# Optimization experiments

Hardware: AMD Instinct MI355X
Metric: run time of the kernel (lower is better)

Reference implementation:

```python
import jax, jax.numpy as jnp
import numpy as np

N_NODES = 100000
N_EDGES = 600000
N_GRAPHS = 5000
IN_DIM = 11
HID = 128
EDGE_DIM = 3
N_REST = 4  # layers 1..4
BN_EPS = 1e-5


def setup_inputs() -> dict:
    key = jax.random.key(0)
    ks = iter(jax.random.split(key, 40))
    s = 0.05
    inp = {}
    inp['x'] = jax.random.normal(next(ks), (N_NODES, IN_DIM), dtype=jnp.float32)
    inp['edge_attr'] = jax.random.normal(next(ks), (N_EDGES, EDGE_DIM), dtype=jnp.float32)
    # layer 0 (input_dim -> hidden)
    inp['e_w0'] = jax.random.normal(next(ks), (EDGE_DIM, IN_DIM), dtype=jnp.float32) * s
    inp['e_b0'] = jnp.zeros((IN_DIM,), jnp.float32)
    inp['w1_0'] = jax.random.normal(next(ks), (IN_DIM, HID), dtype=jnp.float32) * s
    inp['b1_0'] = jnp.zeros((HID,), jnp.float32)
    inp['w2_0'] = jax.random.normal(next(ks), (HID, HID), dtype=jnp.float32) * s
    inp['b2_0'] = jnp.zeros((HID,), jnp.float32)
    inp['gamma0'] = jnp.ones((HID,), jnp.float32)
    inp['beta0'] = jnp.zeros((HID,), jnp.float32)
    inp['eps0'] = jnp.zeros((), jnp.float32)
    # layers 1..4 stacked
    inp['e_w'] = jax.random.normal(next(ks), (N_REST, EDGE_DIM, HID), dtype=jnp.float32) * s
    inp['e_b'] = jnp.zeros((N_REST, HID), jnp.float32)
    inp['w1'] = jax.random.normal(next(ks), (N_REST, HID, HID), dtype=jnp.float32) * s
    inp['b1'] = jnp.zeros((N_REST, HID), jnp.float32)
    inp['w2'] = jax.random.normal(next(ks), (N_REST, HID, HID), dtype=jnp.float32) * s
    inp['b2'] = jnp.zeros((N_REST, HID), jnp.float32)
    inp['gamma'] = jnp.ones((N_REST, HID), jnp.float32)
    inp['beta'] = jnp.zeros((N_REST, HID), jnp.float32)
    inp['eps_r'] = jnp.zeros((N_REST,), jnp.float32)
    # head MLP
    inp['hw1'] = jax.random.normal(next(ks), (HID, HID), dtype=jnp.float32) * s
    inp['hb1'] = jnp.zeros((HID,), jnp.float32)
    inp['hw2'] = jax.random.normal(next(ks), (HID, HID), dtype=jnp.float32) * s
    inp['hb2'] = jnp.zeros((HID,), jnp.float32)
    inp['hw3'] = jax.random.normal(next(ks), (HID, 1), dtype=jnp.float32) * s
    inp['hb3'] = jnp.zeros((1,), jnp.float32)
    # graph structure (int constants)
    inp['edge_index'] = jax.random.randint(next(ks), (2, N_EDGES), 0, N_NODES, dtype=jnp.int32)
    inp['batch'] = jnp.sort(jax.random.randint(next(ks), (N_NODES,), 0, N_GRAPHS, dtype=jnp.int32))
    return inp


def _gine_layer(x, src, dst, edge_attr, e_w, e_b, eps, w1, b1, w2, b2, gamma, beta):
    # message = relu(x_j + Linear(edge_attr)); aggregate = scatter-add on dst
    msg = jax.nn.relu(x[src] + edge_attr @ e_w + e_b)            # [E, d]
    aggr = jax.ops.segment_sum(msg, dst, num_segments=N_NODES)  # [N, d]
    h = (1.0 + eps) * x + aggr
    h = jax.nn.relu(h @ w1 + b1) @ w2 + b2                       # GIN MLP
    mu = h.mean(axis=0)
    var = h.var(axis=0)  # biased, as torch BN training-mode normalization
    h = (h - mu) * jax.lax.rsqrt(var + BN_EPS) * gamma + beta
    return jax.nn.relu(h)


def reference(x, edge_attr, e_w0, e_b0, w1_0, b1_0, w2_0, b2_0, gamma0, beta0, eps0,
              e_w, e_b, w1, b1, w2, b2, gamma, beta, eps_r,
              hw1, hb1, hw2, hb2, hw3, hb3, edge_index, batch):
    src, dst = edge_index[0], edge_index[1]
    # layer 0: input_dim -> hidden, no residual (dims differ)
    h = _gine_layer(x, src, dst, edge_attr, e_w0, e_b0, eps0,
                    w1_0, b1_0, w2_0, b2_0, gamma0, beta0)
    # layers 1..4: hidden -> hidden, with residual
    for i in range(N_REST):
        h_res = h
        h = _gine_layer(h, src, dst, edge_attr, e_w[i], e_b[i], eps_r[i],
                        w1[i], b1[i], w2[i], b2[i], gamma[i], beta[i])
        h = h + h_res
    # global mean pool per graph
    sums = jax.ops.segment_sum(h, batch, num_segments=N_GRAPHS)
    cnts = jax.ops.segment_sum(jnp.ones((h.shape[0],), h.dtype), batch, num_segments=N_GRAPHS)
    pooled = sums / jnp.maximum(cnts, 1.0)[:, None]
    # head MLP (dropout = eval no-op)
    z = jax.nn.relu(pooled @ hw1 + hb1)
    z = jax.nn.relu(z @ hw2 + hb2)
    return z @ hw3 + hb3
```

## Files before the change

kernel.cpp:

```cpp
#include <hip/hip_runtime.h>
#include <hip/hip_fp16.h>

#define N_NODES 100000
#define N_EDGES 600000
#define N_GRAPHS 5000
#define IN_DIM 11
#define HID 128
#define NREST 4
#define BN_EPS 1e-5f
#define SCAN_BS 256
#define NBLK ((N_NODES + SCAN_BS - 1) / SCAN_BS)
#define WSLOT 16384

typedef __bf16 bf16x8 __attribute__((ext_vector_type(8)));
typedef float f32x4 __attribute__((ext_vector_type(4)));

__device__ inline bf16x8 as_bf16x8(uint4 u) { return __builtin_bit_cast(bf16x8, u); }

__device__ inline void split_bf16(float x, unsigned short& hi, unsigned short& lo) {
    unsigned int b = __float_as_uint(x);
    hi = (unsigned short)(b >> 16);
    float rem = x - __uint_as_float(b & 0xFFFF0000u);
    lo = (unsigned short)(__float_as_uint(rem) >> 16);
}

__device__ inline uint4 pack8(const unsigned short* h) {
    uint4 u;
    u.x = (unsigned)h[0] | ((unsigned)h[1] << 16);
    u.y = (unsigned)h[2] | ((unsigned)h[3] << 16);
    u.z = (unsigned)h[4] | ((unsigned)h[5] << 16);
    u.w = (unsigned)h[6] | ((unsigned)h[7] << 16);
    return u;
}

__global__ void k_zero(int* deg, int* gstart, int* gend, float* stats) {
    int i = blockIdx.x * 256 + threadIdx.x;
    if (i < N_NODES) deg[i] = 0;
    if (i < N_GRAPHS) { gstart[i] = 0; gend[i] = 0; }
    if (i < 5 * 2 * HID) stats[i] = 0.f;
}

__global__ void k_deg(const int* __restrict__ ei, int* __restrict__ deg) {
    int e = blockIdx.x * 256 + threadIdx.x;
    if (e < N_EDGES) atomicAdd(&deg[ei[N_EDGES + e]], 1);
}

__global__ void k_scan_a(const int* __restrict__ deg, int* __restrict__ rowstart,
                         int* __restrict__ bsum) {
    __shared__ int sh[SCAN_BS];
    int t = threadIdx.x, i = blockIdx.x * SCAN_BS + t;
    int v = (i < N_NODES) ? deg[i] : 0;
    sh[t] = v;
    __syncthreads();
    for (int off = 1; off < SCAN_BS; off <<= 1) {
        int add = (t >= off) ? sh[t - off] : 0;
        __syncthreads();
        sh[t] += add;
        __syncthreads();
    }
    if (i < N_NODES) rowstart[i] = sh[t] - v;
    if (t == SCAN_BS - 1) bsum[blockIdx.x] = sh[t];
}

__global__ void k_scan_b(const int* __restrict__ bsum, int* __restrict__ boff) {
    __shared__ int sh[512];
    int t = threadIdx.x;
    int v = (t < NBLK) ? bsum[t] : 0;
    sh[t] = v;
    __syncthreads();
    for (int off = 1; off < 512; off <<= 1) {
        int add = (t >= off) ? sh[t - off] : 0;
        __syncthreads();
        sh[t] += add;
        __syncthreads();
    }
    if (t < NBLK) boff[t] = sh[t] - v;
}

__global__ void k_scan_c(int* __restrict__ rowstart, const int* __restrict__ boff,
                         int* __restrict__ cur) {
    int i = blockIdx.x * 256 + threadIdx.x;
    if (i < N_NODES) {
        int v = rowstart[i] + boff[i / SCAN_BS];
        rowstart[i] = v;
        cur[i] = v;
    }
    if (i == 0) rowstart[N_NODES] = N_EDGES;
}

__global__ void k_fill(const int* __restrict__ ei, const float* __restrict__ ea,
                       int* __restrict__ cur, uint4* __restrict__ csr_pack) {
    int e = blockIdx.x * 256 + threadIdx.x;
    if (e < N_EDGES) {
        int d = ei[N_EDGES + e];
        int p = atomicAdd(&cur[d], 1);
        uint4 pk;
        pk.x = (unsigned)ei[e];
        pk.y = __float_as_uint(ea[3 * e + 0]);
        pk.z = __float_as_uint(ea[3 * e + 1]);
        pk.w = __float_as_uint(ea[3 * e + 2]);
        csr_pack[p] = pk;
    }
}

__global__ void k_pack(const float* __restrict__ w1_0, const float* __restrict__ w2_0,
                       const float* __restrict__ w1, const float* __restrict__ w2,
                       unsigned short* __restrict__ Whi, unsigned short* __restrict__ Wlo) {
    int bid = blockIdx.x;
    int slot = bid >> 5;
    int kc = (bid >> 3) & 3, cb = bid & 7;
    int lane = threadIdx.x;
    const float* src;
    int K;
    if (slot == 0) { src = w1_0; K = IN_DIM; }
    else if (slot == 1) { src = w2_0; K = HID; }
    else if (slot < 6) { src = w1 + (size_t)(slot - 2) * HID * HID; K = HID; }
    else { src = w2 + (size_t)(slot - 6) * HID * HID; K = HID; }
    int col = cb * 16 + (lane & 15);
    int kbase = kc * 32 + 8 * (lane >> 4);
    unsigned short hi[8], lo[8];
#pragma unroll
    for (int j = 0; j < 8; ++j) {
        int k = kbase + j;
        float v = (k < K) ? src[(size_t)k * HID + col] : 0.f;
        split_bf16(v, hi[j], lo[j]);
    }
    size_t base = ((size_t)bid * 64 + lane) * 8;
    *(uint4*)(Whi + base) = pack8(hi);
    *(uint4*)(Wlo + base) = pack8(lo);
}

__global__ void k_agg0(const float* __restrict__ x, const int* __restrict__ rowstart,
                       const uint4* __restrict__ csr_pack,
                       const float* __restrict__ ew, const float* __restrict__ eb,
                       const float* __restrict__ epsp, float* __restrict__ Z0) {
    int wave = (blockIdx.x * blockDim.x + threadIdx.x) >> 6;
    int lane = threadIdx.x & 63;
    if (wave >= N_NODES) return;
    int n = wave;
    int slot = lane >> 4;
    int c = lane & 15;
    int cc = (c < IN_DIM) ? c : 0;
    float w0 = ew[cc], w1 = ew[IN_DIM + cc], w2 = ew[2 * IN_DIM + cc];
    float bb = eb[cc];
    float acc = 0.f;
    int i0 = rowstart[n], i1 = rowstart[n + 1];
    int i = i0 + slot;
    uint4 pk;
    if (i < i1) pk = csr_pack[i];
    while (i < i1) {
        int inext = i + 4;
        uint4 pknext;
        if (inext < i1) pknext = csr_pack[inext];
        int s = (int)pk.x;
        float m = x[s * IN_DIM + cc] + __uint_as_float(pk.y) * w0 +
                  __uint_as_float(pk.z) * w1 + __uint_as_float(pk.w) * w2 + bb;
        acc += fmaxf(m, 0.f);
        pk = pknext;
        i = inext;
    }
    acc += __shfl_xor(acc, 16, 64);
    acc += __shfl_xor(acc, 32, 64);
    if (lane < IN_DIM) {
        float epsv = 1.0f + epsp[0];
        Z0[n * IN_DIM + lane] = epsv * x[n * IN_DIM + lane] + acc;
    }
}

__global__ __launch_bounds__(256, 4) void k_agg128(
        const float* __restrict__ h, const __half* __restrict__ hh,
        const int* __restrict__ rowstart, const uint4* __restrict__ csr_pack,
        const float* __restrict__ ew, const float* __restrict__ eb,
        const float* __restrict__ epsp, int layer, float* __restrict__ Z) {
    int wave = (blockIdx.x * blockDim.x + threadIdx.x) >> 6;
    int lane = threadIdx.x & 63;
    if (wave >= N_NODES) return;
    int n = wave;
    int slot = lane >> 4;
    int c = (lane & 15) * 8;
    float4 w0a = *(const float4*)(ew + 0 * HID + c), w0b = *(const float4*)(ew + 0 * HID + c + 4);
    float4 w1a = *(const float4*)(ew + 1 * HID + c), w1b = *(const float4*)(ew + 1 * HID + c + 4);
    float4 w2a = *(const float4*)(ew + 2 * HID + c), w2b = *(const float4*)(ew + 2 * HID + c + 4);
    float4 bba = *(const float4*)(eb + c),           bbb = *(const float4*)(eb + c + 4);
    float a0 = 0.f, a1 = 0.f, a2 = 0.f, a3 = 0.f, a4 = 0.f, a5 = 0.f, a6 = 0.f, a7 = 0.f;
    int i0 = rowstart[n], i1 = rowstart[n + 1];
    int i = i0 + slot;
    uint4 pk;
    if (i < i1) pk = csr_pack[i];
    while (i < i1) {
        int inext = i + 4;
        uint4 pknext;
        if (inext < i1) pknext = csr_pack[inext];
        int s = (int)pk.x;
        float ea0 = __uint_as_float(pk.y);
        float ea1 = __uint_as_float(pk.z);
        float ea2 = __uint_as_float(pk.w);
        uint4 hv = *(const uint4*)(hh + (size_t)s * HID + c);
        float2 f0 = __half22float2(__builtin_bit_cast(__half2, hv.x));
        float2 f1 = __half22float2(__builtin_bit_cast(__half2, hv.y));
        float2 f2 = __half22float2(__builtin_bit_cast(__half2, hv.z));
        float2 f3 = __half22float2(__builtin_bit_cast(__half2, hv.w));
        a0 += fmaxf(f0.x + ea0 * w0a.x + ea1 * w1a.x + ea2 * w2a.x + bba.x, 0.f);
        a1 += fmaxf(f0.y + ea0 * w0a.y + ea1 * w1a.y + ea2 * w2a.y + bba.y, 0.f);
        a2 += fmaxf(f1.x + ea0 * w0a.z + ea1 * w1a.z + ea2 * w2a.z + bba.z, 0.f);
        a3 += fmaxf(f1.y + ea0 * w0a.w + ea1 * w1a.w + ea2 * w2a.w + bba.w, 0.f);
        a4 += fmaxf(f2.x + ea0 * w0b.x + ea1 * w1b.x + ea2 * w2b.x + bbb.x, 0.f);
        a5 += fmaxf(f2.y + ea0 * w0b.y + ea1 * w1b.y + ea2 * w2b.y + bbb.y, 0.f);
        a6 += fmaxf(f3.x + ea0 * w0b.z + ea1 * w1b.z + ea2 * w2b.z + bbb.z, 0.f);
        a7 += fmaxf(f3.y + ea0 * w0b.w + ea1 * w1b.w + ea2 * w2b.w + bbb.w, 0.f);
        pk = pknext;
        i = inext;
    }
#pragma unroll
    for (int m = 16; m <= 32; m <<= 1) {
        a0 += __shfl_xor(a0, m, 64); a1 += __shfl_xor(a1, m, 64);
        a2 += __shfl_xor(a2, m, 64); a3 += __shfl_xor(a3, m, 64);
        a4 += __shfl_xor(a4, m, 64); a5 += __shfl_xor(a5, m, 64);
        a6 += __shfl_xor(a6, m, 64); a7 += __shfl_xor(a7, m, 64);
    }
    if (slot == 0) {
        float epsv = 1.0f + epsp[layer];
        float4 hna = *(const float4*)(h + (size_t)n * HID + c);
        float4 hnb = *(const float4*)(h + (size_t)n * HID + c + 4);
        float4 za, zb;
        za.x = epsv * hna.x + a0; za.y = epsv * hna.y + a1;
        za.z = epsv * hna.z + a2; za.w = epsv * hna.w + a3;
        zb.x = epsv * hnb.x + a4; zb.y = epsv * hnb.y + a5;
        zb.z = epsv * hnb.z + a6; zb.w = epsv * hnb.w + a7;
        *(float4*)(Z + (size_t)n * HID + c) = za;
        *(float4*)(Z + (size_t)n * HID + c + 4) = zb;
    }
}

template <int K1>
__global__ __launch_bounds__(256, 4) void k_mlp(const float* Zin,
        const unsigned short* __restrict__ W1hi, const unsigned short* __restrict__ W1lo,
        const unsigned short* __restrict__ W2hi, const unsigned short* __restrict__ W2lo,
        const float* __restrict__ B1, const float* __restrict__ B2,
        float* Hpre, float* __restrict__ stats) {
    constexpr int KC1 = (K1 == 128) ? 4 : 1;
    __shared__ __align__(16) unsigned short ahi[4 * 4 * 64 * 8];
    __shared__ __align__(16) unsigned short alo[4 * 4 * 64 * 8];
    __shared__ float red[1024];
    const int tid = threadIdx.x;
    const int w = tid >> 6;
    const int l = tid & 63;
    const int row0 = blockIdx.x * 64;

    if (K1 == 128) {
#pragma unroll
        for (int it = 0; it < 4; ++it) {
            int s = tid + it * 256;
            int lane = s & 63, kc = (s >> 6) & 3, wr = s >> 8;
            int r = row0 + wr * 16 + (lane & 15);
            int k0 = kc * 32 + 8 * (lane >> 4);
            float v[8];
            if (r < N_NODES) {
                *(float4*)(v) = *(const float4*)(Zin + (size_t)r * 128 + k0);
                *(float4*)(v + 4) = *(const float4*)(Zin + (size_t)r * 128 + k0 + 4);
            } else {
#pragma unroll
                for (int j = 0; j < 8; ++j) v[j] = 0.f;
            }
            unsigned short h[8], q[8];
#pragma unroll
            for (int j = 0; j < 8; ++j) split_bf16(v[j], h[j], q[j]);
            *(uint4*)(ahi + (size_t)s * 8) = pack8(h);
            *(uint4*)(alo + (size_t)s * 8) = pack8(q);
        }
    } else {
        int lane = tid & 63, wr = tid >> 6;
        int r = row0 + wr * 16 + (lane & 15);
        int k0 = 8 * (lane >> 4);
        float v[8];
#pragma unroll
        for (int j = 0; j < 8; ++j) {
            int k = k0 + j;
            v[j] = (r < N_NODES && k < IN_DIM) ? Zin[(size_t)r * IN_DIM + k] : 0.f;
        }
        unsigned short h[8], q[8];
#pragma unroll
        for (int j = 0; j < 8; ++j) split_bf16(v[j], h[j], q[j]);
        size_t s = (size_t)(wr * 4 + 0) * 64 + lane;
        *(uint4*)(ahi + s * 8) = pack8(h);
        *(uint4*)(alo + s * 8) = pack8(q);
    }
    __syncthreads();

    const int cb0 = 2 * w, cb1 = cb0 + 1;
    const f32x4 zf = {0.f, 0.f, 0.f, 0.f};

    f32x4 acc[4][2];
#pragma unroll
    for (int wr = 0; wr < 4; ++wr) { acc[wr][0] = zf; acc[wr][1] = zf; }

#pragma unroll
    for (int kc = 0; kc < KC1; ++kc) {
        bf16x8 bh0 = as_bf16x8(*(const uint4*)(W1hi + ((size_t)(kc * 8 + cb0) * 64 + l) * 8));
        bf16x8 bl0 = as_bf16x8(*(const uint4*)(W1lo + ((size_t)(kc * 8 + cb0) * 64 + l) * 8));
        bf16x8 bh1 = as_bf16x8(*(const uint4*)(W1hi + ((size_t)(kc * 8 + cb1) * 64 + l) * 8));
        bf16x8 bl1 = as_bf16x8(*(const uint4*)(W1lo + ((size_t)(kc * 8 + cb1) * 64 + l) * 8));
#pragma unroll
        for (int wr = 0; wr < 4; ++wr) {
            bf16x8 a_h = as_bf16x8(*(const uint4*)(ahi + ((size_t)(wr * 4 + kc) * 64 + l) * 8));
            bf16x8 a_l = as_bf16x8(*(const uint4*)(alo + ((size_t)(wr * 4 + kc) * 64 + l) * 8));
            acc[wr][0] = __builtin_amdgcn_mfma_f32_16x16x32_bf16(a_h, bh0, acc[wr][0], 0, 0, 0);
            acc[wr][1] = __builtin_amdgcn_mfma_f32_16x16x32_bf16(a_h, bh1, acc[wr][1], 0, 0, 0);
            acc[wr][0] = __builtin_amdgcn_mfma_f32_16x16x32_bf16(a_l, bh0, acc[wr][0], 0, 0, 0);
            acc[wr][1] = __builtin_amdgcn_mfma_f32_16x16x32_bf16(a_l, bh1, acc[wr][1], 0, 0, 0);
            acc[wr][0] = __builtin_amdgcn_mfma_f32_16x16x32_bf16(a_h, bl0, acc[wr][0], 0, 0, 0);
            acc[wr][1] = __builtin_amdgcn_mfma_f32_16x16x32_bf16(a_h, bl1, acc[wr][1], 0, 0, 0);
        }
    }
    __syncthreads();

    {
        float b1c0 = B1[cb0 * 16 + (l & 15)];
        float b1c1 = B1[cb1 * 16 + (l & 15)];
        int j2 = l & 7;
        int hi16 = (l & 15) >> 3;
        int l2r = (l >> 4) * 4;
#pragma unroll
        for (int wr = 0; wr < 4; ++wr) {
#pragma unroll
            for (int cbl = 0; cbl < 2; ++cbl) {
                float bv = cbl ? b1c1 : b1c0;
                f32x4 v = acc[wr][cbl];
#pragma unroll
                for (int r = 0; r < 4; ++r) {
                    float t = fmaxf(v[r] + bv, 0.f);
                    unsigned short hh, qq;
                    split_bf16(t, hh, qq);
                    int l2 = l2r + r + 16 * (2 * cbl + hi16);
                    int off = ((wr * 4 + w) * 64 + l2) * 8 + j2;
                    ahi[off] = hh;
                    alo[off] = qq;
                }
            }
        }
    }
    __syncthreads();

    f32x4 acc2[4][2];
#pragma unroll
    for (int wr = 0; wr < 4; ++wr) { acc2[wr][0] = zf; acc2[wr][1] = zf; }

#pragma unroll
    for (int kc = 0; kc < 4; ++kc) {
        bf16x8 bh0 = as_bf16x8(*(const uint4*)(W2hi + ((size_t)(kc * 8 + cb0) * 64 + l) * 8));
        bf16x8 bl0 = as_bf16x8(*(const uint4*)(W2lo + ((size_t)(kc * 8 + cb0) * 64 + l) * 8));
        bf16x8 bh1 = as_bf16x8(*(const uint4*)(W2hi + ((size_t)(kc * 8 + cb1) * 64 + l) * 8));
        bf16x8 bl1 = as_bf16x8(*(const uint4*)(W2lo + ((size_t)(kc * 8 + cb1) * 64 + l) * 8));
#pragma unroll
        for (int wr = 0; wr < 4; ++wr) {
            bf16x8 a_h = as_bf16x8(*(const uint4*)(ahi + ((size_t)(wr * 4 + kc) * 64 + l) * 8));
            bf16x8 a_l = as_bf16x8(*(const uint4*)(alo + ((size_t)(wr * 4 + kc) * 64 + l) * 8));
            acc2[wr][0] = __builtin_amdgcn_mfma_f32_16x16x32_bf16(a_h, bh0, acc2[wr][0], 0, 0, 0);
            acc2[wr][1] = __builtin_amdgcn_mfma_f32_16x16x32_bf16(a_h, bh1, acc2[wr][1], 0, 0, 0);
            acc2[wr][0] = __builtin_amdgcn_mfma_f32_16x16x32_bf16(a_l, bh0, acc2[wr][0], 0, 0, 0);
            acc2[wr][1] = __builtin_amdgcn_mfma_f32_16x16x32_bf16(a_l, bh1, acc2[wr][1], 0, 0, 0);
            acc2[wr][0] = __builtin_amdgcn_mfma_f32_16x16x32_bf16(a_h, bl0, acc2[wr][0], 0, 0, 0);
            acc2[wr][1] = __builtin_amdgcn_mfma_f32_16x16x32_bf16(a_h, bl1, acc2[wr][1], 0, 0, 0);
        }
    }

    {
        float b2c0 = B2[cb0 * 16 + (l & 15)];
        float b2c1 = B2[cb1 * 16 + (l & 15)];
        float s0 = 0.f, q0 = 0.f, s1 = 0.f, q1 = 0.f;
#pragma unroll
        for (int wr = 0; wr < 4; ++wr) {
#pragma unroll
            for (int r = 0; r < 4; ++r) {
                int grow = row0 + wr * 16 + (l >> 4) * 4 + r;
                if (grow < N_NODES) {
                    float o0 = acc2[wr][0][r] + b2c0;
                    float o1 = acc2[wr][1][r] + b2c1;
                    Hpre[(size_t)grow * 128 + cb0 * 16 + (l & 15)] = o0;
                    Hpre[(size_t)grow * 128 + cb1 * 16 + (l & 15)] = o1;
                    s0 += o0; q0 += o0 * o0;
                    s1 += o1; q1 += o1 * o1;
                }
            }
        }
        red[(w * 2 + 0) * 64 + l] = s0;
        red[(w * 2 + 1) * 64 + l] = s1;
        red[512 + (w * 2 + 0) * 64 + l] = q0;
        red[512 + (w * 2 + 1) * 64 + l] = q1;
    }
    __syncthreads();
    if (tid < 128) {
        int b = ((tid >> 5) * 2 + ((tid >> 4) & 1)) * 64 + (tid & 15);
        float ss = red[b] + red[b + 16] + red[b + 32] + red[b + 48];
        float qq = red[512 + b] + red[512 + b + 16] + red[512 + b + 32] + red[512 + b + 48];
        atomicAdd(&stats[tid], ss);
        atomicAdd(&stats[128 + tid], qq);
    }
}

__global__ void k_bn(const float* __restrict__ Hpre, const float* __restrict__ stats,
                     const float* __restrict__ gamma, const float* __restrict__ beta,
                     float* __restrict__ h, __half* __restrict__ hh, int residual) {
    int idx = blockIdx.x * 256 + threadIdx.x;
    const float invN = 1.f / (float)N_NODES;
    int c4 = idx & 31;
    float4 v = ((const float4*)Hpre)[idx];
    float4 s0 = ((const float4*)stats)[c4];
    float4 s1 = ((const float4*)(stats + 128))[c4];
    float4 g = ((const float4*)gamma)[c4];
    float4 bt = ((const float4*)beta)[c4];
    float4 r;
    {
        float mu = s0.x * invN, var = s1.x * invN - mu * mu;
        r.x = fmaxf((v.x - mu) * rsqrtf(var + BN_EPS) * g.x + bt.x, 0.f);
    }
    {
        float mu = s0.y * invN, var = s1.y * invN - mu * mu;
        r.y = fmaxf((v.y - mu) * rsqrtf(var + BN_EPS) * g.y + bt.y, 0.f);
    }
    {
        float mu = s0.z * invN, var = s1.z * invN - mu * mu;
        r.z = fmaxf((v.z - mu) * rsqrtf(var + BN_EPS) * g.z + bt.z, 0.f);
    }
    {
        float mu = s0.w * invN, var = s1.w * invN - mu * mu;
        r.w = fmaxf((v.w - mu) * rsqrtf(var + BN_EPS) * g.w + bt.w, 0.f);
    }
    if (residual) {
        float4 hv = ((const float4*)h)[idx];
        r.x += hv.x; r.y += hv.y; r.z += hv.z; r.w += hv.w;
    }
    ((float4*)h)[idx] = r;
    if (hh) {
        __half2 p0 = __floats2half2_rn(r.x, r.y);
        __half2 p1 = __floats2half2_rn(r.z, r.w);
        uint2 pk;
        pk.x = __builtin_bit_cast(unsigned int, p0);
        pk.y = __builtin_bit_cast(unsigned int, p1);
        *(uint2*)(hh + (size_t)idx * 4) = pk;
    }
}

__global__ void k_bounds(const int* __restrict__ batch, int* __restrict__ gstart,
                         int* __restrict__ gend) {
    int r = blockIdx.x * 256 + threadIdx.x;
    if (r >= N_NODES) return;
    int b = batch[r];
    if (r == 0 || batch[r - 1] != b) gstart[b] = r;
    if (r == N_NODES - 1 || batch[r + 1] != b) gend[b] = r + 1;
}

__global__ void k_pool(const float* __restrict__ h, const int* __restrict__ gstart,
                       const int* __restrict__ gend, float* __restrict__ pooled) {
    int wave = (blockIdx.x * blockDim.x + threadIdx.x) >> 6;
    int lane = threadIdx.x & 63;
    if (wave >= N_GRAPHS) return;
    int g = wave;
    int c = lane * 2;
    int a = gstart[g], b = gend[g];
    float ax = 0.f, ay = 0.f;
    for (int r = a; r < b; ++r) {
        float2 v = *(const float2*)(h + (size_t)r * HID + c);
        ax += v.x;
        ay += v.y;
    }
    float d = fmaxf((float)(b - a), 1.f);
    float2 o;
    o.x = ax / d;
    o.y = ay / d;
    *(float2*)(pooled + (size_t)g * HID + c) = o;
}

__global__ void k_head(const float* __restrict__ pooled, const float* __restrict__ hw1,
                       const float* __restrict__ hb1, const float* __restrict__ hw2,
                       const float* __restrict__ hb2, const float* __restrict__ hw3,
                       const float* __restrict__ hb3, float* __restrict__ out) {
    __shared__ float ps[2][128];
    __shared__ float t1s[2][128];
    __shared__ float red[256];
    int tid = threadIdx.x;
    int rr = tid >> 7, c = tid & 127;
    int row = blockIdx.x * 2 + rr;
    ps[rr][c] = pooled[(size_t)row * 128 + c];
    __syncthreads();
    float a = hb1[c];
    for (int k = 0; k < 128; ++k) a = fmaf(ps[rr][k], hw1[k * 128 + c], a);
    t1s[rr][c] = fmaxf(a, 0.f);
    __syncthreads();
    float b = hb2[c];
    for (int k = 0; k < 128; ++k) b = fmaf(t1s[rr][k], hw2[k * 128 + c], b);
    b = fmaxf(b, 0.f);
    red[tid] = b * hw3[c];
    for (int s = 64; s > 0; s >>= 1) {
        __syncthreads();
        if (c < s) red[tid] += red[tid + s];
    }
    __syncthreads();
    if (c == 0) out[row] = red[tid] + hb3[0];
}

extern "C" void kernel_launch(void* const* d_in, const int* in_sizes, int n_in,
                              void* d_out, int out_size, void* d_ws, size_t ws_size,
                              hipStream_t stream) {
    const float* x = (const float*)d_in[0];
    const float* edge_attr = (const float*)d_in[1];
    const float* e_w0 = (const float*)d_in[2];
    const float* e_b0 = (const float*)d_in[3];
    const float* w1_0 = (const float*)d_in[4];
    const float* b1_0 = (const float*)d_in[5];
    const float* w2_0 = (const float*)d_in[6];
    const float* b2_0 = (const float*)d_in[7];
    const float* gamma0 = (const float*)d_in[8];
    const float* beta0 = (const float*)d_in[9];
    const float* eps0 = (const float*)d_in[10];
    const float* e_w = (const float*)d_in[11];
    const float* e_b = (const float*)d_in[12];
    const float* w1 = (const float*)d_in[13];
    const float* b1 = (const float*)d_in[14];
    const float* w2 = (const float*)d_in[15];
    const float* b2 = (const float*)d_in[16];
    const float* gamma = (const float*)d_in[17];
    const float* beta = (const float*)d_in[18];
    const float* eps_r = (const float*)d_in[19];
    const float* hw1 = (const float*)d_in[20];
    const float* hb1 = (const float*)d_in[21];
    const float* hw2 = (const float*)d_in[22];
    const float* hb2 = (const float*)d_in[23];
    const float* hw3 = (const float*)d_in[24];
    const float* hb3 = (const float*)d_in[25];
    const int* edge_index = (const int*)d_in[26];
    const int* batch = (const int*)d_in[27];
    float* out = (float*)d_out;

    float* wsf = (float*)d_ws;
    size_t off = 0;
    float* A = wsf + off;      off += (size_t)N_NODES * HID;
    float* ZB = wsf + off;     off += (size_t)N_NODES * HID;
    float* Z0 = wsf + off;     off += (size_t)N_NODES * IN_DIM;
    float* pooled = wsf + off; off += (size_t)N_GRAPHS * HID;
    float* stats = wsf + off;  off += 5 * 2 * HID;
    __half* hhalf = (__half*)(wsf + off); off += (size_t)N_NODES * HID / 2;
    int* ib = (int*)(wsf + off);
    uint4* csr_pack = (uint4*)ib;
    size_t io = 4 * (size_t)N_EDGES;
    int* deg = ib + io;      io += N_NODES;
    int* rowstart = ib + io; io += N_NODES + 4;
    int* cur = ib + io;      io += N_NODES;
    int* gstart = ib + io;   io += N_GRAPHS;
    int* gend = ib + io;     io += N_GRAPHS;
    int* bsum = ib + io;     io += 512;
    int* boff = ib + io;     io += 512;
    unsigned short* Whi = (unsigned short*)(ib + io);
    unsigned short* Wlo = Whi + 10 * WSLOT;

    const int EB = (N_EDGES + 255) / 256;
    const int NB = (N_NODES + 255) / 256;
    const int MLPB = (N_NODES + 63) / 64;

    k_zero<<<NB, 256, 0, stream>>>(deg, gstart, gend, stats);
    k_pack<<<320, 64, 0, stream>>>(w1_0, w2_0, w1, w2, Whi, Wlo);

    k_deg<<<EB, 256, 0, stream>>>(edge_index, deg);
    k_scan_a<<<NBLK, SCAN_BS, 0, stream>>>(deg, rowstart, bsum);
    k_scan_b<<<1, 512, 0, stream>>>(bsum, boff);
    k_scan_c<<<NB, 256, 0, stream>>>(rowstart, boff, cur);
    k_fill<<<EB, 256, 0, stream>>>(edge_index, edge_attr, cur, csr_pack);

    k_agg0<<<(N_NODES * 64) / 256, 256, 0, stream>>>(x, rowstart, csr_pack, e_w0,
                                                     e_b0, eps0, Z0);
    k_mlp<IN_DIM><<<MLPB, 256, 0, stream>>>(Z0, Whi + 0 * WSLOT, Wlo + 0 * WSLOT,
                                            Whi + 1 * WSLOT, Wlo + 1 * WSLOT,
                                            b1_0, b2_0, ZB, stats);
    k_bn<<<(N_NODES * HID / 4) / 256, 256, 0, stream>>>(ZB, stats, gamma0, beta0, A,
                                                        hhalf, 0);

    for (int i = 0; i < NREST; ++i) {
        k_agg128<<<(N_NODES * 64) / 256, 256, 0, stream>>>(
            A, hhalf, rowstart, csr_pack, e_w + (size_t)i * 3 * HID,
            e_b + (size_t)i * HID, eps_r, i, ZB);
        k_mlp<HID><<<MLPB, 256, 0, stream>>>(ZB, Whi + (size_t)(2 + i) * WSLOT,
                                             Wlo + (size_t)(2 + i) * WSLOT,
                                             Whi + (size_t)(6 + i) * WSLOT,
                                             Wlo + (size_t)(6 + i) * WSLOT,
                                             b1 + (size_t)i * HID, b2 + (size_t)i * HID,
                                             ZB, stats + (size_t)(i + 1) * 2 * HID);
        k_bn<<<(N_NODES * HID / 4) / 256, 256, 0, stream>>>(
            ZB, stats + (size_t)(i + 1) * 2 * HID, gamma + (size_t)i * HID,
            beta + (size_t)i * HID, A, (i < NREST - 1) ? hhalf : (__half*)nullptr, 1);
    }

    k_bounds<<<NB, 256, 0, stream>>>(batch, gstart, gend);
    k_pool<<<(N_GRAPHS * 64) / 256, 256, 0, stream>>>(A, gstart, gend, pooled);
    k_head<<<N_GRAPHS / 2, 256, 0, stream>>>(pooled, hw1, hb1, hw2, hb2, hw3, hb3, out);
}
```

Before: 920.3 us.

## Store node features only in fp16, ping-pong buffers, drop fp32 copy

Removes the fp32 node-feature buffer. k_bn now writes only fp16 output, reads the fp16 residual from the previous buffer, and processes 8 elements per thread. k_agg128 and k_pool read the self term and pooled values from fp16, and two fp16 buffers alternate between layers. The manual software prefetch in the aggregation loops is replaced with plain loops. This cuts the memory traffic of BN, the self read and pooling, but carrying the residual stream in fp16 lets rounding error build up across layers.

```diff
diff --git a/kernel.cpp b/kernel.cpp
--- a/kernel.cpp
+++ b/kernel.cpp
@@ -145,19 +145,12 @@
     float bb = eb[cc];
     float acc = 0.f;
     int i0 = rowstart[n], i1 = rowstart[n + 1];
-    int i = i0 + slot;
-    uint4 pk;
-    if (i < i1) pk = csr_pack[i];
-    while (i < i1) {
-        int inext = i + 4;
-        uint4 pknext;
-        if (inext < i1) pknext = csr_pack[inext];
+    for (int i = i0 + slot; i < i1; i += 4) {
+        uint4 pk = csr_pack[i];
         int s = (int)pk.x;
         float m = x[s * IN_DIM + cc] + __uint_as_float(pk.y) * w0 +
                   __uint_as_float(pk.z) * w1 + __uint_as_float(pk.w) * w2 + bb;
         acc += fmaxf(m, 0.f);
-        pk = pknext;
-        i = inext;
     }
     acc += __shfl_xor(acc, 16, 64);
     acc += __shfl_xor(acc, 32, 64);
@@ -168,8 +161,8 @@
 }
 
 __global__ __launch_bounds__(256, 4) void k_agg128(
-        const float* __restrict__ h, const __half* __restrict__ hh,
-        const int* __restrict__ rowstart, const uint4* __restrict__ csr_pack,
+        const __half* __restrict__ hh, const int* __restrict__ rowstart,
+        const uint4* __restrict__ csr_pack,
         const float* __restrict__ ew, const float* __restrict__ eb,
         const float* __restrict__ epsp, int layer, float* __restrict__ Z) {
     int wave = (blockIdx.x * blockDim.x + threadIdx.x) >> 6;
@@ -184,13 +177,8 @@
     float4 bba = *(const float4*)(eb + c),           bbb = *(const float4*)(eb + c + 4);
     float a0 = 0.f, a1 = 0.f, a2 = 0.f, a3 = 0.f, a4 = 0.f, a5 = 0.f, a6 = 0.f, a7 = 0.f;
     int i0 = rowstart[n], i1 = rowstart[n + 1];
-    int i = i0 + slot;
-    uint4 pk;
-    if (i < i1) pk = csr_pack[i];
-    while (i < i1) {
-        int inext = i + 4;
-        uint4 pknext;
-        if (inext < i1) pknext = csr_pack[inext];
+    for (int i = i0 + slot; i < i1; i += 4) {
+        uint4 pk = csr_pack[i];
         int s = (int)pk.x;
         float ea0 = __uint_as_float(pk.y);
         float ea1 = __uint_as_float(pk.z);
@@ -208,8 +196,6 @@
         a5 += fmaxf(f2.y + ea0 * w0b.y + ea1 * w1b.y + ea2 * w2b.y + bbb.y, 0.f);
         a6 += fmaxf(f3.x + ea0 * w0b.z + ea1 * w1b.z + ea2 * w2b.z + bbb.z, 0.f);
         a7 += fmaxf(f3.y + ea0 * w0b.w + ea1 * w1b.w + ea2 * w2b.w + bbb.w, 0.f);
-        pk = pknext;
-        i = inext;
     }
 #pragma unroll
     for (int m = 16; m <= 32; m <<= 1) {
@@ -220,13 +206,16 @@
     }
     if (slot == 0) {
         float epsv = 1.0f + epsp[layer];
-        float4 hna = *(const float4*)(h + (size_t)n * HID + c);
-        float4 hnb = *(const float4*)(h + (size_t)n * HID + c + 4);
+        uint4 hv = *(const uint4*)(hh + (size_t)n * HID + c);
+        float2 f0 = __half22float2(__builtin_bit_cast(__half2, hv.x));
+        float2 f1 = __half22float2(__builtin_bit_cast(__half2, hv.y));
+        float2 f2 = __half22float2(__builtin_bit_cast(__half2, hv.z));
+        float2 f3 = __half22float2(__builtin_bit_cast(__half2, hv.w));
         float4 za, zb;
-        za.x = epsv * hna.x + a0; za.y = epsv * hna.y + a1;
-        za.z = epsv * hna.z + a2; za.w = epsv * hna.w + a3;
-        zb.x = epsv * hnb.x + a4; zb.y = epsv * hnb.y + a5;
-        zb.z = epsv * hnb.z + a6; zb.w = epsv * hnb.w + a7;
+        za.x = epsv * f0.x + a0; za.y = epsv * f0.y + a1;
+        za.z = epsv * f1.x + a2; za.w = epsv * f1.y + a3;
+        zb.x = epsv * f2.x + a4; zb.y = epsv * f2.y + a5;
+        zb.z = epsv * f3.x + a6; zb.w = epsv * f3.y + a7;
         *(float4*)(Z + (size_t)n * HID + c) = za;
         *(float4*)(Z + (size_t)n * HID + c + 4) = zb;
     }
@@ -400,45 +389,47 @@
 
 __global__ void k_bn(const float* __restrict__ Hpre, const float* __restrict__ stats,
                      const float* __restrict__ gamma, const float* __restrict__ beta,
-                     float* __restrict__ h, __half* __restrict__ hh, int residual) {
+                     const __half* __restrict__ hprev, __half* __restrict__ hout) {
     int idx = blockIdx.x * 256 + threadIdx.x;
     const float invN = 1.f / (float)N_NODES;
-    int c4 = idx & 31;
-    float4 v = ((const float4*)Hpre)[idx];
-    float4 s0 = ((const float4*)stats)[c4];
-    float4 s1 = ((const float4*)(stats + 128))[c4];
-    float4 g = ((const float4*)gamma)[c4];
-    float4 bt = ((const float4*)beta)[c4];
-    float4 r;
-    {
-        float mu = s0.x * invN, var = s1.x * invN - mu * mu;
-        r.x = fmaxf((v.x - mu) * rsqrtf(var + BN_EPS) * g.x + bt.x, 0.f);
-    }
-    {
-        float mu = s0.y * invN, var = s1.y * invN - mu * mu;
-        r.y = fmaxf((v.y - mu) * rsqrtf(var + BN_EPS) * g.y + bt.y, 0.f);
-    }
-    {
-        float mu = s0.z * invN, var = s1.z * invN - mu * mu;
-        r.z = fmaxf((v.z - mu) * rsqrtf(var + BN_EPS) * g.z + bt.z, 0.f);
-    }
-    {
-        float mu = s0.w * invN, var = s1.w * invN - mu * mu;
-        r.w = fmaxf((v.w - mu) * rsqrtf(var + BN_EPS) * g.w + bt.w, 0.f);
-    }
-    if (residual) {
-        float4 hv = ((const float4*)h)[idx];
-        r.x += hv.x; r.y += hv.y; r.z += hv.z; r.w += hv.w;
-    }
-    ((float4*)h)[idx] = r;
-    if (hh) {
-        __half2 p0 = __floats2half2_rn(r.x, r.y);
-        __half2 p1 = __floats2half2_rn(r.z, r.w);
-        uint2 pk;
-        pk.x = __builtin_bit_cast(unsigned int, p0);
-        pk.y = __builtin_bit_cast(unsigned int, p1);
-        *(uint2*)(hh + (size_t)idx * 4) = pk;
-    }
+    int cg = (idx & 15) * 8;
+    const float* hp = Hpre + (size_t)idx * 8;
+    float4 v0 = *(const float4*)(hp);
+    float4 v1 = *(const float4*)(hp + 4);
+    float4 s0a = *(const float4*)(stats + cg);
+    float4 s0b = *(const float4*)(stats + cg + 4);
+    float4 s1a = *(const float4*)(stats + 128 + cg);
+    float4 s1b = *(const float4*)(stats + 128 + cg + 4);
+    float4 ga = *(const float4*)(gamma + cg);
+    float4 gb = *(const float4*)(gamma + cg + 4);
+    float4 ba = *(const float4*)(beta + cg);
+    float4 bb = *(const float4*)(beta + cg + 4);
+    float vv[8] = {v0.x, v0.y, v0.z, v0.w, v1.x, v1.y, v1.z, v1.w};
+    float sm[8] = {s0a.x, s0a.y, s0a.z, s0a.w, s0b.x, s0b.y, s0b.z, s0b.w};
+    float sq[8] = {s1a.x, s1a.y, s1a.z, s1a.w, s1b.x, s1b.y, s1b.z, s1b.w};
+    float gg[8] = {ga.x, ga.y, ga.z, ga.w, gb.x, gb.y, gb.z, gb.w};
+    float be[8] = {ba.x, ba.y, ba.z, ba.w, bb.x, bb.y, bb.z, bb.w};
+    float o[8];
+#pragma unroll
+    for (int j = 0; j < 8; ++j) {
+        float mu = sm[j] * invN, var = sq[j] * invN - mu * mu;
+        o[j] = fmaxf((vv[j] - mu) * rsqrtf(var + BN_EPS) * gg[j] + be[j], 0.f);
+    }
+    if (hprev) {
+        uint4 pv = *(const uint4*)(hprev + (size_t)idx * 8);
+        float2 r0 = __half22float2(__builtin_bit_cast(__half2, pv.x));
+        float2 r1 = __half22float2(__builtin_bit_cast(__half2, pv.y));
+        float2 r2 = __half22float2(__builtin_bit_cast(__half2, pv.z));
+        float2 r3 = __half22float2(__builtin_bit_cast(__half2, pv.w));
+        o[0] += r0.x; o[1] += r0.y; o[2] += r1.x; o[3] += r1.y;
+        o[4] += r2.x; o[5] += r2.y; o[6] += r3.x; o[7] += r3.y;
+    }
+    uint4 st;
+    st.x = __builtin_bit_cast(unsigned int, __floats2half2_rn(o[0], o[1]));
+    st.y = __builtin_bit_cast(unsigned int, __floats2half2_rn(o[2], o[3]));
+    st.z = __builtin_bit_cast(unsigned int, __floats2half2_rn(o[4], o[5]));
+    st.w = __builtin_bit_cast(unsigned int, __floats2half2_rn(o[6], o[7]));
+    *(uint4*)(hout + (size_t)idx * 8) = st;
 }
 
 __global__ void k_bounds(const int* __restrict__ batch, int* __restrict__ gstart,
@@ -450,7 +441,7 @@
     if (r == N_NODES - 1 || batch[r + 1] != b) gend[b] = r + 1;
 }
 
-__global__ void k_pool(const float* __restrict__ h, const int* __restrict__ gstart,
+__global__ void k_pool(const __half* __restrict__ hh, const int* __restrict__ gstart,
                        const int* __restrict__ gend, float* __restrict__ pooled) {
     int wave = (blockIdx.x * blockDim.x + threadIdx.x) >> 6;
     int lane = threadIdx.x & 63;
@@ -460,9 +451,10 @@
     int a = gstart[g], b = gend[g];
     float ax = 0.f, ay = 0.f;
     for (int r = a; r < b; ++r) {
-        float2 v = *(const float2*)(h + (size_t)r * HID + c);
-        ax += v.x;
-        ay += v.y;
+        __half2 v = *(const __half2*)(hh + (size_t)r * HID + c);
+        float2 f = __half22float2(v);
+        ax += f.x;
+        ay += f.y;
     }
     float d = fmaxf((float)(b - a), 1.f);
     float2 o;
@@ -534,12 +526,12 @@
 
     float* wsf = (float*)d_ws;
     size_t off = 0;
-    float* A = wsf + off;      off += (size_t)N_NODES * HID;
     float* ZB = wsf + off;     off += (size_t)N_NODES * HID;
-    float* Z0 = wsf + off;     off += (size_t)N_NODES * IN_DIM;
+    float* Z0 = wsf + off;     off += (size_t)N_NODES * IN_DIM + 4;
     float* pooled = wsf + off; off += (size_t)N_GRAPHS * HID;
     float* stats = wsf + off;  off += 5 * 2 * HID;
-    __half* hhalf = (__half*)(wsf + off); off += (size_t)N_NODES * HID / 2;
+    __half* hhA = (__half*)(wsf + off); off += (size_t)N_NODES * HID / 2;
+    __half* hhB = (__half*)(wsf + off); off += (size_t)N_NODES * HID / 2;
     int* ib = (int*)(wsf + off);
     uint4* csr_pack = (uint4*)ib;
     size_t io = 4 * (size_t)N_EDGES;
@@ -556,6 +548,7 @@
     const int EB = (N_EDGES + 255) / 256;
     const int NB = (N_NODES + 255) / 256;
     const int MLPB = (N_NODES + 63) / 64;
+    const int BNB = (N_NODES * HID / 8) / 256;
 
     k_zero<<<NB, 256, 0, stream>>>(deg, gstart, gend, stats);
     k_pack<<<320, 64, 0, stream>>>(w1_0, w2_0, w1, w2, Whi, Wlo);
@@ -571,12 +564,13 @@
     k_mlp<IN_DIM><<<MLPB, 256, 0, stream>>>(Z0, Whi + 0 * WSLOT, Wlo + 0 * WSLOT,
                                             Whi + 1 * WSLOT, Wlo + 1 * WSLOT,
                                             b1_0, b2_0, ZB, stats);
-    k_bn<<<(N_NODES * HID / 4) / 256, 256, 0, stream>>>(ZB, stats, gamma0, beta0, A,
-                                                        hhalf, 0);
-
+    k_bn<<<BNB, 256, 0, stream>>>(ZB, stats, gamma0, beta0, (const __half*)nullptr, hhA);
+
+    __half* hcur = hhA;
+    __half* hnxt = hhB;
     for (int i = 0; i < NREST; ++i) {
         k_agg128<<<(N_NODES * 64) / 256, 256, 0, stream>>>(
-            A, hhalf, rowstart, csr_pack, e_w + (size_t)i * 3 * HID,
+            hcur, rowstart, csr_pack, e_w + (size_t)i * 3 * HID,
             e_b + (size_t)i * HID, eps_r, i, ZB);
         k_mlp<HID><<<MLPB, 256, 0, stream>>>(ZB, Whi + (size_t)(2 + i) * WSLOT,
                                              Wlo + (size_t)(2 + i) * WSLOT,
@@ -584,12 +578,13 @@
                                              Wlo + (size_t)(6 + i) * WSLOT,
                                              b1 + (size_t)i * HID, b2 + (size_t)i * HID,
                                              ZB, stats + (size_t)(i + 1) * 2 * HID);
-        k_bn<<<(N_NODES * HID / 4) / 256, 256, 0, stream>>>(
-            ZB, stats + (size_t)(i + 1) * 2 * HID, gamma + (size_t)i * HID,
-            beta + (size_t)i * HID, A, (i < NREST - 1) ? hhalf : (__half*)nullptr, 1);
+        k_bn<<<BNB, 256, 0, stream>>>(ZB, stats + (size_t)(i + 1) * 2 * HID,
+                                      gamma + (size_t)i * HID, beta + (size_t)i * HID,
+                                      hcur, hnxt);
+        __half* t = hcur; hcur = hnxt; hnxt = t;
     }
 
     k_bounds<<<NB, 256, 0, stream>>>(batch, gstart, gend);
-    k_pool<<<(N_GRAPHS * 64) / 256, 256, 0, stream>>>(A, gstart, gend, pooled);
+    k_pool<<<(N_GRAPHS * 64) / 256, 256, 0, stream>>>(hcur, gstart, gend, pooled);
     k_head<<<N_GRAPHS / 2, 256, 0, stream>>>(pooled, hw1, hb1, hw2, hb2, hw3, hb3, out);
 }
```

Measured after the change: 940.4 us. +2.2%, slower.
